# Optimization experiments

Measured on AMD Instinct MI355X. Metric: run time of the kernel, lower is better.

Reference implementation:

```python
import jax, jax.numpy as jnp
import numpy as np

# irreps_in == irreps_out == 512x0e + 256x1o + 128x2e
# each entry: (multiplicity, irrep dimension 2l+1)
IRREPS = [(512, 1), (256, 3), (128, 5)]
DIM_TOTAL = sum(m * d for m, d in IRREPS)          # 1920
WEIGHT_NUMEL = sum(m * m for m, _ in IRREPS)       # 344064
N = 16384


def setup_inputs() -> dict:
    key = jax.random.key(0)
    kx, kw = jax.random.split(key)
    x = jax.random.normal(kx, (N, DIM_TOTAL), dtype=jnp.float32)
    weight = jax.random.normal(kw, (WEIGHT_NUMEL,), dtype=jnp.float32)
    return {"x": x, "weight": weight}


def reference(x, weight):
    """Segmented (block-diagonal per irrep) linear mixing with 1/sqrt(fan_in) norm."""
    n = x.shape[0]
    outs = []
    x_off = 0
    w_off = 0
    for mul, d in IRREPS:
        seg = x[:, x_off:x_off + mul * d].reshape(n, mul, d)      # [N, mul, 2l+1]
        W = weight[w_off:w_off + mul * mul].reshape(mul, mul)     # [mul_in, mul_out]
        scale = jnp.asarray(1.0 / np.sqrt(mul), dtype=x.dtype)
        y = jnp.einsum('nui,uv->nvi', seg, W) * scale             # channel mix per component
        outs.append(y.reshape(n, mul * d))
        x_off += mul * d
        w_off += mul * mul
    return jnp.concatenate(outs, axis=-1)
```

## Files before the change

kernel.cpp:

```cpp
#include <hip/hip_runtime.h>
#include <hip/hip_bf16.h>


typedef float  f32x4  __attribute__((ext_vector_type(4)));
typedef short  bf16x8 __attribute__((ext_vector_type(8)));

#define ROWLEN 1920

__device__ __forceinline__ unsigned short f2bf(float f) {
    union { float f; unsigned int u; } c; c.f = f;
    unsigned int u = c.u;
    u += 0x7fffu + ((u >> 16) & 1u);
    return (unsigned short)(u >> 16);
}

__global__ __launch_bounds__(256) void prep_weights(const float* __restrict__ w,
                                                    unsigned short* __restrict__ wt) {
    int g = blockIdx.x * 256 + threadIdx.x;
    if (g >= 344064) return;
    int base, sh;
    if      (g < 262144) { base = 0;      sh = 9; }
    else if (g < 327680) { base = 262144; sh = 8; }
    else                 { base = 327680; sh = 7; }
    int local = g - base;
    int u = local >> sh;
    int v = local & ((1 << sh) - 1);
    wt[base + (v << sh) + u] = f2bf(w[g]);
}

template<int MUL, int D, int TN, int X_OFF, int WT_BASE>
__global__ __launch_bounds__(256) void seg_gemm(const float* __restrict__ x,
                                                const unsigned short* __restrict__ wt,
                                                float* __restrict__ out,
                                                float scale) {
    constexpr int KB      = 32;
    constexpr int NSTEP   = MUL / KB;
    constexpr int M_LOG   = TN * D;
    constexpr int MT      = M_LOG / 16;
    constexpr int WAVE_NT = MUL / 64;
    constexpr int STRIDE  = KB + 8;
    constexpr int ROW_F   = KB * D;
    constexpr int ROW_F4  = ROW_F / 4;
    constexpr int TOT_F4  = TN * ROW_F4;

    __shared__ unsigned short lds[M_LOG * STRIDE];

    const int tid  = threadIdx.x;
    const int wave = tid >> 6;
    const int lane = tid & 63;
    const int q    = lane >> 4;
    const int t16  = lane & 15;
    const int n0   = blockIdx.x * TN;

    f32x4 acc[MT][WAVE_NT];
#pragma unroll
    for (int a = 0; a < MT; ++a)
#pragma unroll
        for (int b = 0; b < WAVE_NT; ++b) acc[a][b] = (f32x4)0.0f;

    const float* __restrict__ xblk = x + X_OFF + n0 * ROWLEN;
    const unsigned short* __restrict__ wblk = wt + WT_BASE;
    const int vbase = wave * (WAVE_NT * 16) + t16;

    for (int ks = 0; ks < NSTEP; ++ks) {
        const int u0 = ks * KB;
        __syncthreads();
        for (int idx = tid; idx < TOT_F4; idx += 256) {
            const int nl = idx / ROW_F4;
            const int c4 = (idx % ROW_F4) * 4;
            const f32x4 vv = *(const f32x4*)(xblk + nl * ROWLEN + u0 * D + c4);
            if (D == 1) {
                unsigned int lo = f2bf(vv[0]) | ((unsigned int)f2bf(vv[1]) << 16);
                unsigned int hi = f2bf(vv[2]) | ((unsigned int)f2bf(vv[3]) << 16);
                unsigned int* p = (unsigned int*)&lds[nl * STRIDE + c4];
                p[0] = lo; p[1] = hi;
            } else {
#pragma unroll
                for (int e = 0; e < 4; ++e) {
                    const int c = c4 + e;
                    const int u = c / D;
                    const int i = c % D;
                    lds[(i * TN + nl) * STRIDE + u] = f2bf(vv[e]);
                }
            }
        }
        __syncthreads();
        bf16x8 afr[MT];
#pragma unroll
        for (int tm = 0; tm < MT; ++tm)
            afr[tm] = *(const bf16x8*)&lds[(16 * tm + t16) * STRIDE + q * 8];
#pragma unroll
        for (int tv = 0; tv < WAVE_NT; ++tv) {
            const bf16x8 bfr = *(const bf16x8*)&wblk[(vbase + tv * 16) * MUL + u0 + q * 8];
#pragma unroll
            for (int tm = 0; tm < MT; ++tm)
                acc[tm][tv] = __builtin_amdgcn_mfma_f32_16x16x32_bf16(afr[tm], bfr, acc[tm][tv], 0, 0, 0);
        }
    }

#pragma unroll
    for (int tm = 0; tm < MT; ++tm) {
#pragma unroll
        for (int tv = 0; tv < WAVE_NT; ++tv) {
            const int v = vbase + tv * 16;
#pragma unroll
            for (int r = 0; r < 4; ++r) {
                const int rit = q * 4 + r;
                const int nl   = (D == 1) ? (16 * tm + rit) : rit;
                const int comp = (D == 1) ? 0 : tm;
                out[(n0 + nl) * ROWLEN + X_OFF + v * D + comp] = acc[tm][tv][r] * scale;
            }
        }
    }
}

extern "C" void kernel_launch(void* const* d_in, const int* in_sizes, int n_in,
                              void* d_out, int out_size, void* d_ws, size_t ws_size,
                              hipStream_t stream) {
    const float* x = (const float*)d_in[0];
    const float* w = (const float*)d_in[1];
    float* out = (float*)d_out;
    unsigned short* wt = (unsigned short*)d_ws;

    hipLaunchKernelGGL(prep_weights, dim3((344064 + 255) / 256), dim3(256), 0, stream, w, wt);

    hipLaunchKernelGGL((seg_gemm<512, 1, 32, 0, 0>),
                       dim3(16384 / 32), dim3(256), 0, stream, x, wt, out, 0.044194173824f);
    hipLaunchKernelGGL((seg_gemm<256, 3, 16, 512, 262144>),
                       dim3(16384 / 16), dim3(256), 0, stream, x, wt, out, 0.0625f);
    hipLaunchKernelGGL((seg_gemm<128, 5, 16, 1280, 327680>),
                       dim3(16384 / 16), dim3(256), 0, stream, x, wt, out, 0.088388347648f);
}
```

Before: 292.8 us.

## Stage full K-extent of x tile into LDS once, removing per-step barriers

```diff
diff --git a/kernel.cpp b/kernel.cpp
--- a/kernel.cpp
+++ b/kernel.cpp
@@ -33,15 +33,12 @@
                                                 const unsigned short* __restrict__ wt,
                                                 float* __restrict__ out,
                                                 float scale) {
-    constexpr int KB      = 32;
-    constexpr int NSTEP   = MUL / KB;
+    constexpr int NSTEP   = MUL / 32;
     constexpr int M_LOG   = TN * D;
     constexpr int MT      = M_LOG / 16;
     constexpr int WAVE_NT = MUL / 64;
-    constexpr int STRIDE  = KB + 8;
-    constexpr int ROW_F   = KB * D;
-    constexpr int ROW_F4  = ROW_F / 4;
-    constexpr int TOT_F4  = TN * ROW_F4;
+    constexpr int STRIDE  = MUL + 8;
+    constexpr int NUG     = MUL / 8;
 
     __shared__ unsigned short lds[M_LOG * STRIDE];
 
@@ -52,43 +49,44 @@
     const int t16  = lane & 15;
     const int n0   = blockIdx.x * TN;
 
+    const float* __restrict__ xblk = x + X_OFF + n0 * ROWLEN;
+    const unsigned short* __restrict__ wblk = wt + WT_BASE;
+
+    for (int idx = tid; idx < TN * NUG; idx += 256) {
+        const int nl = idx / NUG;
+        const int ug = idx % NUG;
+        const float* src = xblk + nl * ROWLEN + ug * 8 * D;
+        f32x4 v[2 * D];
+#pragma unroll
+        for (int j = 0; j < 2 * D; ++j) v[j] = *(const f32x4*)(src + 4 * j);
+#pragma unroll
+        for (int i = 0; i < D; ++i) {
+            bf16x8 o;
+#pragma unroll
+            for (int t = 0; t < 8; ++t) {
+                const int j = t * D + i;
+                o[t] = (short)f2bf(v[j >> 2][j & 3]);
+            }
+            *(bf16x8*)&lds[(i * TN + nl) * STRIDE + ug * 8] = o;
+        }
+    }
+    __syncthreads();
+
     f32x4 acc[MT][WAVE_NT];
 #pragma unroll
     for (int a = 0; a < MT; ++a)
 #pragma unroll
         for (int b = 0; b < WAVE_NT; ++b) acc[a][b] = (f32x4)0.0f;
 
-    const float* __restrict__ xblk = x + X_OFF + n0 * ROWLEN;
-    const unsigned short* __restrict__ wblk = wt + WT_BASE;
     const int vbase = wave * (WAVE_NT * 16) + t16;
 
+#pragma unroll
     for (int ks = 0; ks < NSTEP; ++ks) {
-        const int u0 = ks * KB;
-        __syncthreads();
-        for (int idx = tid; idx < TOT_F4; idx += 256) {
-            const int nl = idx / ROW_F4;
-            const int c4 = (idx % ROW_F4) * 4;
-            const f32x4 vv = *(const f32x4*)(xblk + nl * ROWLEN + u0 * D + c4);
-            if (D == 1) {
-                unsigned int lo = f2bf(vv[0]) | ((unsigned int)f2bf(vv[1]) << 16);
-                unsigned int hi = f2bf(vv[2]) | ((unsigned int)f2bf(vv[3]) << 16);
-                unsigned int* p = (unsigned int*)&lds[nl * STRIDE + c4];
-                p[0] = lo; p[1] = hi;
-            } else {
-#pragma unroll
-                for (int e = 0; e < 4; ++e) {
-                    const int c = c4 + e;
-                    const int u = c / D;
-                    const int i = c % D;
-                    lds[(i * TN + nl) * STRIDE + u] = f2bf(vv[e]);
-                }
-            }
-        }
-        __syncthreads();
+        const int u0 = ks * 32;
         bf16x8 afr[MT];
 #pragma unroll
         for (int tm = 0; tm < MT; ++tm)
-            afr[tm] = *(const bf16x8*)&lds[(16 * tm + t16) * STRIDE + q * 8];
+            afr[tm] = *(const bf16x8*)&lds[(16 * tm + t16) * STRIDE + u0 + q * 8];
 #pragma unroll
         for (int tv = 0; tv < WAVE_NT; ++tv) {
             const bf16x8 bfr = *(const bf16x8*)&wblk[(vbase + tv * 16) * MUL + u0 + q * 8];
```

Measured after the change: 296.3 us. About the same (+1.2%).
